# Optimization experiments

Measured on AMD Instinct MI355X. Metric: run time of the kernel, lower is better.

## Reference

```python
import jax, jax.numpy as jnp
import numpy as np

B, N, D = 2, 2048, 1024
H, WS = 16, 128  # num_heads, window_size
DH = D // H
HALF = WS // 2  # window is [i-HALF, i+HALF] inclusive -> 129 keys interior


def setup_inputs() -> dict:
    key = jax.random.key(0)
    ks = jax.random.split(key, 5)
    return {
        "x": jax.random.normal(ks[0], (B, N, D), dtype=jnp.float32),
        "Wqkv": jax.random.normal(ks[1], (D, 3 * D), dtype=jnp.float32) * 0.02,
        "bqkv": jax.random.normal(ks[2], (3 * D,), dtype=jnp.float32) * 0.02,
        "Wout": jax.random.normal(ks[3], (D, D), dtype=jnp.float32) * 0.02,
        "bout": jax.random.normal(ks[4], (D,), dtype=jnp.float32) * 0.02,
    }


def reference(x, Wqkv, bqkv, Wout, bout):
    b, n, d = x.shape
    scale = DH ** -0.5
    qkv = x @ Wqkv + bqkv  # [b, n, 3d]
    q, k, v = jnp.split(qkv, 3, axis=-1)
    # [b, n, d] -> [b, h, n, dh]
    def heads(t):
        return t.reshape(b, n, H, DH).transpose(0, 2, 1, 3)
    q, k, v = heads(q), heads(k), heads(v)
    scores = jnp.einsum("bhid,bhjd->bhij", q, k) * scale  # [b, h, n, n]
    # per-token window [max(0,i-HALF), min(n,i+HALF+1)) == |i-j| <= HALF
    idx = jnp.arange(n)
    band = jnp.abs(idx[:, None] - idx[None, :]) <= HALF  # [n, n]
    neg = jnp.asarray(jnp.finfo(scores.dtype).min, scores.dtype)
    scores = jnp.where(band[None, None], scores, neg)
    attn = jax.nn.softmax(scores, axis=-1)
    out = jnp.einsum("bhij,bhjd->bhid", attn, v)  # [b, h, n, dh]
    out = out.transpose(0, 2, 1, 3).reshape(b, n, d)
    return out @ Wout + bout
```

## Files before the change

kernel.cpp:

```cpp
#include <hip/hip_runtime.h>
#include <hip/hip_bf16.h>
#include <cstdint>
#include <cstddef>

#define BB 2
#define NN 2048
#define DD 1024
#define HH 16
#define DHH 64
#define SCALE 0.125f

typedef _Float16 f16x8 __attribute__((ext_vector_type(8)));
typedef _Float16 f16x4 __attribute__((ext_vector_type(4)));
typedef float f32x4 __attribute__((ext_vector_type(4)));

#define AS1(p) ((__attribute__((address_space(1))) void*)(p))
#define AS3(p) ((__attribute__((address_space(3))) void*)(p))

__global__ __launch_bounds__(256) void prep(const float* __restrict__ x, _Float16* __restrict__ x_h,
                                            const float* __restrict__ Wqkv, _Float16* __restrict__ Wqkv_t,
                                            const float* __restrict__ Wout, _Float16* __restrict__ Wout_t) {
    __shared__ float tile[32][33];
    int bx = blockIdx.x, tid = threadIdx.x;
    if (bx < 2048) {
        int i = bx * 2048 + tid * 8;
        f32x4 a = *(const f32x4*)(x + i);
        f32x4 b = *(const f32x4*)(x + i + 4);
        f16x8 o;
        o[0] = (_Float16)a[0]; o[1] = (_Float16)a[1]; o[2] = (_Float16)a[2]; o[3] = (_Float16)a[3];
        o[4] = (_Float16)b[0]; o[5] = (_Float16)b[1]; o[6] = (_Float16)b[2]; o[7] = (_Float16)b[3];
        *(f16x8*)(x_h + i) = o;
        return;
    }
    const float* in; _Float16* out; int C, tc, tr;
    if (bx < 5120) { int t = bx - 2048; C = 3 * DD; in = Wqkv; out = Wqkv_t; tc = t % 96; tr = t / 96; }
    else           { int t = bx - 5120; C = DD;     in = Wout; out = Wout_t; tc = t % 32; tr = t / 32; }
    int R = DD;
    int txx = tid & 31, ty = tid >> 5;
    int r0 = tr * 32, c0 = tc * 32;
#pragma unroll
    for (int i = 0; i < 32; i += 8)
        tile[ty + i][txx] = in[(size_t)(r0 + ty + i) * C + (c0 + txx)];
    __syncthreads();
#pragma unroll
    for (int i = 0; i < 32; i += 8)
        out[(size_t)(c0 + ty + i) * R + (r0 + txx)] = (_Float16)tile[txx][ty + i];
}

template <bool SWAP, int MT>
__device__ __forceinline__ void gemm_kloop(const _Float16* __restrict__ gA,
                                           const _Float16* __restrict__ gB,
                                           _Float16* lA, _Float16* lB,
                                           const _Float16* As, const _Float16* Bs,
                                           int wm, int wn, int llo, int lhi, int K,
                                           f32x4 acc[][MT > 4 ? MT : 4]) {
    for (int k0 = 0; k0 < K; k0 += 64) {
        __syncthreads();
#pragma unroll
        for (int p = 0; p < MT; ++p)
            __builtin_amdgcn_global_load_lds(AS1(gA + (size_t)p * 8 * K + k0), AS3(lA + p * 512), 16, 0, 0);
#pragma unroll
        for (int p = 0; p < 4; ++p)
            __builtin_amdgcn_global_load_lds(AS1(gB + (size_t)p * 8 * K + k0), AS3(lB + p * 512), 16, 0, 0);
        __syncthreads();

#pragma unroll
        for (int ks = 0; ks < 2; ++ks) {
            f16x8 af[MT], bf[4];
            int swz = (((ks * 4 + lhi) ^ (llo & 7)) * 8);
#pragma unroll
            for (int mt = 0; mt < MT; ++mt)
                af[mt] = *(const f16x8*)(As + (wm + mt * 16 + llo) * 64 + swz);
#pragma unroll
            for (int nt = 0; nt < 4; ++nt)
                bf[nt] = *(const f16x8*)(Bs + (wn + nt * 16 + llo) * 64 + swz);
            if (SWAP) {
#pragma unroll
                for (int nt = 0; nt < 4; ++nt)
#pragma unroll
                    for (int mt = 0; mt < MT; ++mt)
                        acc[nt][mt] = __builtin_amdgcn_mfma_f32_16x16x32_f16(bf[nt], af[mt], acc[nt][mt], 0, 0, 0);
            } else {
#pragma unroll
                for (int mt = 0; mt < MT; ++mt)
#pragma unroll
                    for (int nt = 0; nt < 4; ++nt)
                        acc[mt][nt] = __builtin_amdgcn_mfma_f32_16x16x32_f16(af[mt], bf[nt], acc[mt][nt], 0, 0, 0);
            }
        }
    }
}

template <bool SWAP>
__device__ __forceinline__ void qkv_body(const _Float16* __restrict__ A,
                                         const _Float16* __restrict__ Bt,
                                         const float* __restrict__ bias,
                                         _Float16* __restrict__ q_h,
                                         _Float16* __restrict__ k_h,
                                         _Float16* __restrict__ vt_h,
                                         _Float16* As, _Float16* Bs,
                                         int bm, int bn, int region) {
    (void)region;
    int tid = threadIdx.x;
    int wave = tid >> 6, lane = tid & 63;
    int llo = lane & 15, lhi = lane >> 4;
    int wm = (wave >> 2) * 128, wn = (wave & 3) * 64;
    int l8 = lane >> 3;
    int gchunk = ((lane & 7) ^ l8) * 8;

    int rAu = wm + (wave & 3) * 16;
    int rBu = (wave >> 1) * 64 + (wave & 1) * 16;
    const _Float16* gA = A + (size_t)(bm + rAu + l8) * DD + gchunk;
    const _Float16* gB = Bt + (size_t)(bn + rBu + l8) * DD + gchunk;
    _Float16* lA = As + rAu * 64 + lane * 8;
    _Float16* lB = Bs + rBu * 64 + lane * 8;

#define STA(H, C, T, U) __builtin_amdgcn_global_load_lds( \
        AS1(gA + (size_t)((H) * 64 + (C) * 8) * DD + (T) * 64), \
        AS3(lA + (U) * 16384 + ((H) * 64 + (C) * 8) * 64), 16, 0, 0)
#define STB(H, C, T, U) __builtin_amdgcn_global_load_lds( \
        AS1(gB + (size_t)((H) * 32 + (C) * 8) * DD + (T) * 64), \
        AS3(lB + (U) * 16384 + ((H) * 32 + (C) * 8) * 64), 16, 0, 0)
#define RDA(MT, KS, U) (*(const f16x8*)(As + (U) * 16384 + (wm + (MT) * 16 + llo) * 64 + ((((KS) * 4 + lhi) ^ (llo & 7)) * 8)))
#define RDB(NT, KS, U) (*(const f16x8*)(Bs + (U) * 16384 + (wn + (NT) * 16 + llo) * 64 + ((((KS) * 4 + lhi) ^ (llo & 7)) * 8)))
#define MM(MT, NT, KS) do { \
        if constexpr (SWAP) acc[NT][MT] = __builtin_amdgcn_mfma_f32_16x16x32_f16(bf[NT][KS], af[(MT) & 3][KS], acc[NT][MT], 0, 0, 0); \
        else acc[MT][NT] = __builtin_amdgcn_mfma_f32_16x16x32_f16(af[(MT) & 3][KS], bf[NT][KS], acc[MT][NT], 0, 0, 0); \
    } while (0)

    f32x4 acc[SWAP ? 4 : 8][SWAP ? 8 : 4] = {};
    f16x8 af[4][2], bf[4][2];

    STA(0, 0, 0, 0); STA(0, 1, 0, 0);
    STB(0, 0, 0, 0); STB(0, 1, 0, 0);
    STB(1, 0, 0, 0); STB(1, 1, 0, 0);
    STA(1, 0, 0, 0); STA(1, 1, 0, 0);
    asm volatile("s_waitcnt vmcnt(2)" ::: "memory");
    __builtin_amdgcn_s_barrier();

#pragma unroll 1
    for (int t = 0; t < 15; ++t) {
        int u = t & 1, nu = u ^ 1;
#pragma unroll
        for (int mt = 0; mt < 4; ++mt) { af[mt][0] = RDA(mt, 0, u); af[mt][1] = RDA(mt, 1, u); }
#pragma unroll
        for (int nt = 0; nt < 4; ++nt) { bf[nt][0] = RDB(nt, 0, u); bf[nt][1] = RDB(nt, 1, u); }
        STA(0, 0, t + 1, nu); STA(0, 1, t + 1, nu);
        STB(0, 0, t + 1, nu); STB(0, 1, t + 1, nu);
        STB(1, 0, t + 1, nu); STB(1, 1, t + 1, nu);
        __builtin_amdgcn_s_barrier();
        asm volatile("s_waitcnt lgkmcnt(0)" ::: "memory");
        __builtin_amdgcn_s_setprio(1);
#pragma unroll
        for (int ks = 0; ks < 2; ++ks)
#pragma unroll
            for (int mt = 0; mt < 4; ++mt) { MM(mt, 0, ks); MM(mt, 1, ks); MM(mt, 2, ks); MM(mt, 3, ks); }
        __builtin_amdgcn_s_setprio(0);
        asm volatile("s_waitcnt vmcnt(6)" ::: "memory");
        __builtin_amdgcn_s_barrier();
#pragma unroll
        for (int mt = 0; mt < 4; ++mt) { af[mt][0] = RDA(mt + 4, 0, u); af[mt][1] = RDA(mt + 4, 1, u); }
        STA(1, 0, t + 1, nu); STA(1, 1, t + 1, nu);
        __builtin_amdgcn_s_barrier();
        asm volatile("s_waitcnt lgkmcnt(0)" ::: "memory");
        __builtin_amdgcn_s_setprio(1);
#pragma unroll
        for (int ks = 0; ks < 2; ++ks)
#pragma unroll
            for (int mt = 4; mt < 8; ++mt) { MM(mt, 0, ks); MM(mt, 1, ks); MM(mt, 2, ks); MM(mt, 3, ks); }
        __builtin_amdgcn_s_setprio(0);
        asm volatile("s_waitcnt vmcnt(2)" ::: "memory");
        __builtin_amdgcn_s_barrier();
    }

    {
#pragma unroll
        for (int mt = 0; mt < 4; ++mt) { af[mt][0] = RDA(mt, 0, 1); af[mt][1] = RDA(mt, 1, 1); }
#pragma unroll
        for (int nt = 0; nt < 4; ++nt) { bf[nt][0] = RDB(nt, 0, 1); bf[nt][1] = RDB(nt, 1, 1); }
        asm volatile("s_waitcnt lgkmcnt(0)" ::: "memory");
        __builtin_amdgcn_s_setprio(1);
#pragma unroll
        for (int ks = 0; ks < 2; ++ks)
#pragma unroll
            for (int mt = 0; mt < 4; ++mt) { MM(mt, 0, ks); MM(mt, 1, ks); MM(mt, 2, ks); MM(mt, 3, ks); }
        __builtin_amdgcn_s_setprio(0);
        asm volatile("s_waitcnt vmcnt(0)" ::: "memory");
        __builtin_amdgcn_s_barrier();
#pragma unroll
        for (int mt = 0; mt < 4; ++mt) { af[mt][0] = RDA(mt + 4, 0, 1); af[mt][1] = RDA(mt + 4, 1, 1); }
        asm volatile("s_waitcnt lgkmcnt(0)" ::: "memory");
        __builtin_amdgcn_s_setprio(1);
#pragma unroll
        for (int ks = 0; ks < 2; ++ks)
#pragma unroll
            for (int mt = 4; mt < 8; ++mt) { MM(mt, 0, ks); MM(mt, 1, ks); MM(mt, 2, ks); MM(mt, 3, ks); }
        __builtin_amdgcn_s_setprio(0);
    }

    __builtin_amdgcn_s_barrier();
    _Float16* R = (wave < 4) ? (As + wave * 8192) : (Bs + (wave - 4) * 8192);
    int bq = bm >> 11;
    int nb = (bm & 2047) + wm;

    if constexpr (SWAP) {
#pragma unroll
        for (int nt = 0; nt < 4; ++nt) {
            int fb = nt * 16 + lhi * 4;
            f32x4 b4 = *(const f32x4*)(bias + bn + wn + fb);
            int chunk = fb >> 3, off = fb & 7;
#pragma unroll
            for (int mt = 0; mt < 8; ++mt) {
                int t = mt * 16 + llo;
                f16x4 v4;
#pragma unroll
                for (int r = 0; r < 4; ++r) v4[r] = (_Float16)(acc[nt][mt][r] + b4[r]);
                *(f16x4*)(R + t * 64 + ((chunk ^ (t & 7)) << 3) + off) = v4;
            }
        }
        asm volatile("s_waitcnt lgkmcnt(0)" ::: "memory");
        _Float16* dst0 = (region == 0 ? q_h : k_h);
        int cb = (bn & 1023) + wn;
#pragma unroll
        for (int it = 0; it < 16; ++it) {
            int t = it * 8 + l8;
            f16x8 v = *(const f16x8*)(R + t * 64 + (((lane & 7) ^ (t & 7)) << 3));
            *(f16x8*)(dst0 + (size_t)(bq * NN + nb + t) * DD + cb + (lane & 7) * 8) = v;
        }
    } else {
#pragma unroll
        for (int nt = 0; nt < 4; ++nt) {
            int f = nt * 16 + llo;
            float bv = bias[bn + wn + f];
#pragma unroll
            for (int mt = 0; mt < 8; ++mt) {
                int tb = mt * 16 + lhi * 4;
                int chunk = tb >> 3, off = tb & 7;
                int slot = (chunk & 8) | ((chunk & 7) ^ (f & 7));
                f16x4 v4;
#pragma unroll
                for (int r = 0; r < 4; ++r) v4[r] = (_Float16)(acc[mt][nt][r] + bv);
                *(f16x4*)(R + f * 128 + (slot << 3) + off) = v4;
            }
        }
        asm volatile("s_waitcnt lgkmcnt(0)" ::: "memory");
        int cb = (bn & 1023) + wn;
#pragma unroll
        for (int it = 0; it < 16; ++it) {
            int f = it * 4 + lhi;
            int chunk = llo;
            int slot = (chunk & 8) | ((chunk & 7) ^ (f & 7));
            f16x8 v = *(const f16x8*)(R + f * 128 + (slot << 3));
            int c = cb + f;
            int h = c >> 6, dh = c & 63;
            *(f16x8*)(vt_h + ((size_t)((bq * HH + h) * DHH + dh)) * NN + nb + chunk * 8) = v;
        }
    }
#undef STA
#undef STB
#undef RDA
#undef RDB
#undef MM
}

__global__ __launch_bounds__(512, 2) void gemm_qkv(const _Float16* __restrict__ A,
                                                   const _Float16* __restrict__ Bt,
                                                   const float* __restrict__ bias,
                                                   _Float16* __restrict__ q_h,
                                                   _Float16* __restrict__ k_h,
                                                   _Float16* __restrict__ vt_h) {
    __shared__ __align__(16) _Float16 As[2 * 16384];
    __shared__ __align__(16) _Float16 Bs[2 * 16384];
    int id = blockIdx.x;
    int xcd = id & 7, jj = id >> 3;
    int mtile = (xcd >> 1) * 4 + jj / 6;
    int ntile = (xcd & 1) * 6 + jj % 6;
    int bm = mtile * 256, bn = ntile * 256;
    int region = bn >> 10;
    if (region == 2)
        qkv_body<false>(A, Bt, bias, q_h, k_h, vt_h, As, Bs, bm, bn, region);
    else
        qkv_body<true>(A, Bt, bias, q_h, k_h, vt_h, As, Bs, bm, bn, region);
}

__global__ __launch_bounds__(256) void gemm_out(const _Float16* __restrict__ A,
                                                const _Float16* __restrict__ Bt,
                                                const float* __restrict__ bias,
                                                float* __restrict__ Cf) {
    const int K = DD, N = DD;
    __shared__ __align__(16) _Float16 As[128 * 64];
    __shared__ __align__(16) _Float16 Bs[128 * 64];
    int id = blockIdx.x;
    int xcd = id & 7, j = id >> 3;
    int bm = (xcd * 4 + (j >> 3)) * 128;
    int bn = (j & 7) * 128;
    int tid = threadIdx.x;
    int wave = tid >> 6, lane = tid & 63;
    int wm = (wave >> 1) * 64, wn = (wave & 1) * 64;
    int lhi = lane >> 4, llo = lane & 15;

    f32x4 acc[4][4] = {};

    int srow = wave * 32 + (lane >> 3);
    int scol = ((lane & 7) ^ (lane >> 3)) * 8;
    const _Float16* gA = A + (size_t)(bm + srow) * K + scol;
    const _Float16* gB = Bt + (size_t)(bn + srow) * K + scol;
    _Float16* lA = As + wave * 2048 + lane * 8;
    _Float16* lB = Bs + wave * 2048 + lane * 8;

    gemm_kloop<true, 4>(gA, gB, lA, lB, As, Bs, wm, wn, llo, lhi, K, acc);

#pragma unroll
    for (int nt = 0; nt < 4; ++nt) {
        int cbase = bn + wn + nt * 16 + lhi * 4;
        f32x4 b4 = *(const f32x4*)(bias + cbase);
#pragma unroll
        for (int mt = 0; mt < 4; ++mt) {
            int t = bm + wm + mt * 16 + llo;
            f32x4 v4;
#pragma unroll
            for (int r = 0; r < 4; ++r) v4[r] = acc[nt][mt][r] + b4[r];
            *(f32x4*)(Cf + (size_t)t * N + cbase) = v4;
        }
    }
}

#define KP 64
#define PP 200
#define VP 200
__global__ __launch_bounds__(256) void local_attn(const _Float16* __restrict__ q_h,
                                                  const _Float16* __restrict__ k_h,
                                                  const _Float16* __restrict__ vt_h,
                                                  _Float16* __restrict__ outh) {
    __shared__ __align__(16) _Float16 KsPs[64 * PP];
    __shared__ __align__(16) _Float16 Vt[64 * VP];
    _Float16* Ks = KsPs;
    _Float16* Ps = KsPs;
    int tid = threadIdx.x;
    int id = blockIdx.x;
    int xcd = id & 7, j = id >> 3;
    int i0 = (xcd * 4 + (j & 3)) * 64;
    int hb = j >> 2;
    int h = hb & 15, b = hb >> 4;

    int wave = tid >> 6, lane = tid & 63;
    int llo = lane & 15, lhi = lane >> 4;

    {
        int srow = lane >> 3;
        int chunk = ((lane & 7) ^ (lane >> 3)) * 8;
        const _Float16* kb = k_h + (size_t)(b * NN) * DD + h * DHH + chunk;
#pragma unroll
        for (int q = 0; q < 6; ++q) {
            int p = wave * 6 + q;
            int jj = i0 - 64 + p * 8 + srow;
            __builtin_amdgcn_global_load_lds(AS1(kb + (ptrdiff_t)jj * DD), AS3(Ks + p * 512 + lane * 8), 16, 0, 0);
        }
    }

    {
        const _Float16* vb = vt_h + (size_t)((b * HH + h) * DHH) * NN + (i0 - 64);
        for (int u = tid; u < 1536; u += 256) {
            int d = u / 24, c = u % 24;
            f16x8 vv = *(const f16x8*)(vb + (ptrdiff_t)d * NN + c * 8);
            *(f16x8*)(Vt + d * VP + c * 8) = vv;
        }
    }

    int qrow = wave * 16 + llo;
    int qi = i0 + qrow;
    const _Float16* qp = q_h + (size_t)(b * NN + qi) * DD + h * DHH;
    f16x8 qf0 = *(const f16x8*)(qp + lhi * 8);
    f16x8 qf1 = *(const f16x8*)(qp + 32 + lhi * 8);
    __syncthreads();

    float sc[12][4];
#pragma unroll
    for (int mt = 0; mt < 12; ++mt) {
        const _Float16* kr = Ks + (mt * 16 + llo) * 64;
        f16x8 kf0 = *(const f16x8*)(kr + ((lhi ^ (llo & 7)) * 8));
        f16x8 kf1 = *(const f16x8*)(kr + (((lhi + 4) ^ (llo & 7)) * 8));
        f32x4 a = {0.f, 0.f, 0.f, 0.f};
        a = __builtin_amdgcn_mfma_f32_16x16x32_f16(kf0, qf0, a, 0, 0, 0);
        a = __builtin_amdgcn_mfma_f32_16x16x32_f16(kf1, qf1, a, 0, 0, 0);
#pragma unroll
        for (int r = 0; r < 4; ++r) sc[mt][r] = a[r];
    }
    __syncthreads();

    float m = -1e30f;
#pragma unroll
    for (int mt = 0; mt < 12; ++mt)
#pragma unroll
        for (int r = 0; r < 4; ++r) {
            int sidx = mt * 16 + lhi * 4 + r;
            int jj = i0 - 64 + sidx;
            int dj = jj - qi;
            bool valid = (jj >= 0) && (jj < NN) && (dj <= 64) && (dj >= -64);
            float v = valid ? sc[mt][r] * SCALE : -1e30f;
            sc[mt][r] = v;
            m = fmaxf(m, v);
        }
    m = fmaxf(m, __shfl_xor(m, 16, 64));
    m = fmaxf(m, __shfl_xor(m, 32, 64));
    float l = 0.f;
#pragma unroll
    for (int mt = 0; mt < 12; ++mt)
#pragma unroll
        for (int r = 0; r < 4; ++r) {
            float e = __expf(sc[mt][r] - m);
            sc[mt][r] = e;
            l += e;
        }
    l += __shfl_xor(l, 16, 64);
    l += __shfl_xor(l, 32, 64);
    float invl = 1.f / l;

#pragma unroll
    for (int mt = 0; mt < 12; ++mt) {
        f16x4 pv;
#pragma unroll
        for (int r = 0; r < 4; ++r) pv[r] = (_Float16)(sc[mt][r] * invl);
        *(f16x4*)(Ps + qrow * PP + mt * 16 + lhi * 4) = pv;
    }
    __asm__ volatile("s_waitcnt lgkmcnt(0)" ::: "memory");

    f32x4 oacc[4] = {};
#pragma unroll
    for (int ks = 0; ks < 6; ++ks) {
        f16x8 pf = *(const f16x8*)(Ps + (wave * 16 + llo) * PP + ks * 32 + lhi * 8);
#pragma unroll
        for (int nt = 0; nt < 4; ++nt) {
            f16x8 vf = *(const f16x8*)(Vt + (nt * 16 + llo) * VP + ks * 32 + lhi * 8);
            oacc[nt] = __builtin_amdgcn_mfma_f32_16x16x32_f16(pf, vf, oacc[nt], 0, 0, 0);
        }
    }

    _Float16* orow = outh + (size_t)(b * NN) * DD + h * DHH;
#pragma unroll
    for (int nt = 0; nt < 4; ++nt)
#pragma unroll
        for (int r = 0; r < 4; ++r) {
            int q = wave * 16 + lhi * 4 + r;
            int d = nt * 16 + llo;
            orow[(size_t)(i0 + q) * DD + d] = (_Float16)oacc[nt][r];
        }
}

extern "C" void kernel_launch(void* const* d_in, const int* in_sizes, int n_in,
                              void* d_out, int out_size, void* d_ws, size_t ws_size,
                              hipStream_t stream) {
    const float* x    = (const float*)d_in[0];
    const float* Wqkv = (const float*)d_in[1];
    const float* bqkv = (const float*)d_in[2];
    const float* Wout = (const float*)d_in[3];
    const float* bout = (const float*)d_in[4];
    float* out = (float*)d_out;

    char* ws = (char*)d_ws;
    _Float16* x_h    = (_Float16*)(ws);
    _Float16* Wqkv_t = (_Float16*)(ws + (size_t)8  * 1024 * 1024);
    _Float16* Wout_t = (_Float16*)(ws + (size_t)14 * 1024 * 1024);
    _Float16* q_h    = (_Float16*)(ws + (size_t)16 * 1024 * 1024);
    _Float16* k_h    = (_Float16*)(ws + (size_t)24 * 1024 * 1024);
    _Float16* vt_h   = (_Float16*)(ws + (size_t)32 * 1024 * 1024);
    _Float16* attn_h = (_Float16*)(ws + (size_t)40 * 1024 * 1024);

    prep<<<6144, 256, 0, stream>>>(x, x_h, Wqkv, Wqkv_t, Wout, Wout_t);

    gemm_qkv<<<192, 512, 0, stream>>>(x_h, Wqkv_t, bqkv, q_h, k_h, vt_h);

    local_attn<<<1024, 256, 0, stream>>>(q_h, k_h, vt_h, attn_h);

    gemm_out<<<256, 256, 0, stream>>>(attn_h, Wout_t, bout, out);
}
```

Before: 151.8 us.

## Fuse all four stages into one cooperative persistent kernel with grid syncs

Replaces the four separate launches (prep, QKV GEMM, local attention, output GEMM) with one cooperative kernel of 256 blocks of 512 threads, using grid.sync between stages. This removes per-launch overhead and inter-kernel gaps. The attention tile is reshaped to 128 queries per block, with each wave working on only its 9 relevant key tiles instead of 12, and the output GEMM is retiled for 512 threads. The costs are fewer resident blocks during the element-wise and attention stages, idle blocks during the QKV stage (only 192 of 256 work), and the latency of grid-wide barriers.

```diff
diff --git a/kernel.cpp b/kernel.cpp
--- a/kernel.cpp
+++ b/kernel.cpp
@@ -1,7 +1,10 @@
 #include <hip/hip_runtime.h>
+#include <hip/hip_cooperative_groups.h>
 #include <hip/hip_bf16.h>
 #include <cstdint>
 #include <cstddef>
+
+namespace cg = cooperative_groups;
 
 #define BB 2
 #define NN 2048
@@ -16,80 +19,6 @@
 
 #define AS1(p) ((__attribute__((address_space(1))) void*)(p))
 #define AS3(p) ((__attribute__((address_space(3))) void*)(p))
-
-__global__ __launch_bounds__(256) void prep(const float* __restrict__ x, _Float16* __restrict__ x_h,
-                                            const float* __restrict__ Wqkv, _Float16* __restrict__ Wqkv_t,
-                                            const float* __restrict__ Wout, _Float16* __restrict__ Wout_t) {
-    __shared__ float tile[32][33];
-    int bx = blockIdx.x, tid = threadIdx.x;
-    if (bx < 2048) {
-        int i = bx * 2048 + tid * 8;
-        f32x4 a = *(const f32x4*)(x + i);
-        f32x4 b = *(const f32x4*)(x + i + 4);
-        f16x8 o;
-        o[0] = (_Float16)a[0]; o[1] = (_Float16)a[1]; o[2] = (_Float16)a[2]; o[3] = (_Float16)a[3];
-        o[4] = (_Float16)b[0]; o[5] = (_Float16)b[1]; o[6] = (_Float16)b[2]; o[7] = (_Float16)b[3];
-        *(f16x8*)(x_h + i) = o;
-        return;
-    }
-    const float* in; _Float16* out; int C, tc, tr;
-    if (bx < 5120) { int t = bx - 2048; C = 3 * DD; in = Wqkv; out = Wqkv_t; tc = t % 96; tr = t / 96; }
-    else           { int t = bx - 5120; C = DD;     in = Wout; out = Wout_t; tc = t % 32; tr = t / 32; }
-    int R = DD;
-    int txx = tid & 31, ty = tid >> 5;
-    int r0 = tr * 32, c0 = tc * 32;
-#pragma unroll
-    for (int i = 0; i < 32; i += 8)
-        tile[ty + i][txx] = in[(size_t)(r0 + ty + i) * C + (c0 + txx)];
-    __syncthreads();
-#pragma unroll
-    for (int i = 0; i < 32; i += 8)
-        out[(size_t)(c0 + ty + i) * R + (r0 + txx)] = (_Float16)tile[txx][ty + i];
-}
-
-template <bool SWAP, int MT>
-__device__ __forceinline__ void gemm_kloop(const _Float16* __restrict__ gA,
-                                           const _Float16* __restrict__ gB,
-                                           _Float16* lA, _Float16* lB,
-                                           const _Float16* As, const _Float16* Bs,
-                                           int wm, int wn, int llo, int lhi, int K,
-                                           f32x4 acc[][MT > 4 ? MT : 4]) {
-    for (int k0 = 0; k0 < K; k0 += 64) {
-        __syncthreads();
-#pragma unroll
-        for (int p = 0; p < MT; ++p)
-            __builtin_amdgcn_global_load_lds(AS1(gA + (size_t)p * 8 * K + k0), AS3(lA + p * 512), 16, 0, 0);
-#pragma unroll
-        for (int p = 0; p < 4; ++p)
-            __builtin_amdgcn_global_load_lds(AS1(gB + (size_t)p * 8 * K + k0), AS3(lB + p * 512), 16, 0, 0);
-        __syncthreads();
-
-#pragma unroll
-        for (int ks = 0; ks < 2; ++ks) {
-            f16x8 af[MT], bf[4];
-            int swz = (((ks * 4 + lhi) ^ (llo & 7)) * 8);
-#pragma unroll
-            for (int mt = 0; mt < MT; ++mt)
-                af[mt] = *(const f16x8*)(As + (wm + mt * 16 + llo) * 64 + swz);
-#pragma unroll
-            for (int nt = 0; nt < 4; ++nt)
-                bf[nt] = *(const f16x8*)(Bs + (wn + nt * 16 + llo) * 64 + swz);
-            if (SWAP) {
-#pragma unroll
-                for (int nt = 0; nt < 4; ++nt)
-#pragma unroll
-                    for (int mt = 0; mt < MT; ++mt)
-                        acc[nt][mt] = __builtin_amdgcn_mfma_f32_16x16x32_f16(bf[nt], af[mt], acc[nt][mt], 0, 0, 0);
-            } else {
-#pragma unroll
-                for (int mt = 0; mt < MT; ++mt)
-#pragma unroll
-                    for (int nt = 0; nt < 4; ++nt)
-                        acc[mt][nt] = __builtin_amdgcn_mfma_f32_16x16x32_f16(af[mt], bf[nt], acc[mt][nt], 0, 0, 0);
-            }
-        }
-    }
-}
 
 template <bool SWAP>
 __device__ __forceinline__ void qkv_body(const _Float16* __restrict__ A,
@@ -263,84 +192,20 @@
 #undef MM
 }
 
-__global__ __launch_bounds__(512, 2) void gemm_qkv(const _Float16* __restrict__ A,
-                                                   const _Float16* __restrict__ Bt,
-                                                   const float* __restrict__ bias,
-                                                   _Float16* __restrict__ q_h,
-                                                   _Float16* __restrict__ k_h,
-                                                   _Float16* __restrict__ vt_h) {
-    __shared__ __align__(16) _Float16 As[2 * 16384];
-    __shared__ __align__(16) _Float16 Bs[2 * 16384];
-    int id = blockIdx.x;
-    int xcd = id & 7, jj = id >> 3;
-    int mtile = (xcd >> 1) * 4 + jj / 6;
-    int ntile = (xcd & 1) * 6 + jj % 6;
-    int bm = mtile * 256, bn = ntile * 256;
-    int region = bn >> 10;
-    if (region == 2)
-        qkv_body<false>(A, Bt, bias, q_h, k_h, vt_h, As, Bs, bm, bn, region);
-    else
-        qkv_body<true>(A, Bt, bias, q_h, k_h, vt_h, As, Bs, bm, bn, region);
-}
-
-__global__ __launch_bounds__(256) void gemm_out(const _Float16* __restrict__ A,
-                                                const _Float16* __restrict__ Bt,
-                                                const float* __restrict__ bias,
-                                                float* __restrict__ Cf) {
-    const int K = DD, N = DD;
-    __shared__ __align__(16) _Float16 As[128 * 64];
-    __shared__ __align__(16) _Float16 Bs[128 * 64];
-    int id = blockIdx.x;
+#define PP2 168
+#define VP2 280
+__device__ __forceinline__ void attn_tile(int id, _Float16* smem,
+                                          const _Float16* __restrict__ q_h,
+                                          const _Float16* __restrict__ k_h,
+                                          const _Float16* __restrict__ vt_h,
+                                          _Float16* __restrict__ outh) {
+    _Float16* Ks = smem;
+    _Float16* Ps = smem;
+    _Float16* Vt = smem + 21504;
+    int tid = threadIdx.x;
     int xcd = id & 7, j = id >> 3;
-    int bm = (xcd * 4 + (j >> 3)) * 128;
-    int bn = (j & 7) * 128;
-    int tid = threadIdx.x;
-    int wave = tid >> 6, lane = tid & 63;
-    int wm = (wave >> 1) * 64, wn = (wave & 1) * 64;
-    int lhi = lane >> 4, llo = lane & 15;
-
-    f32x4 acc[4][4] = {};
-
-    int srow = wave * 32 + (lane >> 3);
-    int scol = ((lane & 7) ^ (lane >> 3)) * 8;
-    const _Float16* gA = A + (size_t)(bm + srow) * K + scol;
-    const _Float16* gB = Bt + (size_t)(bn + srow) * K + scol;
-    _Float16* lA = As + wave * 2048 + lane * 8;
-    _Float16* lB = Bs + wave * 2048 + lane * 8;
-
-    gemm_kloop<true, 4>(gA, gB, lA, lB, As, Bs, wm, wn, llo, lhi, K, acc);
-
-#pragma unroll
-    for (int nt = 0; nt < 4; ++nt) {
-        int cbase = bn + wn + nt * 16 + lhi * 4;
-        f32x4 b4 = *(const f32x4*)(bias + cbase);
-#pragma unroll
-        for (int mt = 0; mt < 4; ++mt) {
-            int t = bm + wm + mt * 16 + llo;
-            f32x4 v4;
-#pragma unroll
-            for (int r = 0; r < 4; ++r) v4[r] = acc[nt][mt][r] + b4[r];
-            *(f32x4*)(Cf + (size_t)t * N + cbase) = v4;
-        }
-    }
-}
-
-#define KP 64
-#define PP 200
-#define VP 200
-__global__ __launch_bounds__(256) void local_attn(const _Float16* __restrict__ q_h,
-                                                  const _Float16* __restrict__ k_h,
-                                                  const _Float16* __restrict__ vt_h,
-                                                  _Float16* __restrict__ outh) {
-    __shared__ __align__(16) _Float16 KsPs[64 * PP];
-    __shared__ __align__(16) _Float16 Vt[64 * VP];
-    _Float16* Ks = KsPs;
-    _Float16* Ps = KsPs;
-    int tid = threadIdx.x;
-    int id = blockIdx.x;
-    int xcd = id & 7, j = id >> 3;
-    int i0 = (xcd * 4 + (j & 3)) * 64;
-    int hb = j >> 2;
+    int i0 = (xcd * 2 + (j & 1)) * 128;
+    int hb = j >> 1;
     int h = hb & 15, b = hb >> 4;
 
     int wave = tid >> 6, lane = tid & 63;
@@ -351,8 +216,8 @@
         int chunk = ((lane & 7) ^ (lane >> 3)) * 8;
         const _Float16* kb = k_h + (size_t)(b * NN) * DD + h * DHH + chunk;
 #pragma unroll
-        for (int q = 0; q < 6; ++q) {
-            int p = wave * 6 + q;
+        for (int q = 0; q < 4; ++q) {
+            int p = wave * 4 + q;
             int jj = i0 - 64 + p * 8 + srow;
             __builtin_amdgcn_global_load_lds(AS1(kb + (ptrdiff_t)jj * DD), AS3(Ks + p * 512 + lane * 8), 16, 0, 0);
         }
@@ -360,10 +225,16 @@
 
     {
         const _Float16* vb = vt_h + (size_t)((b * HH + h) * DHH) * NN + (i0 - 64);
-        for (int u = tid; u < 1536; u += 256) {
-            int d = u / 24, c = u % 24;
+#pragma unroll
+        for (int u = tid; u < 2048; u += 512) {
+            int d = u >> 5, c = u & 31;
             f16x8 vv = *(const f16x8*)(vb + (ptrdiff_t)d * NN + c * 8);
-            *(f16x8*)(Vt + d * VP + c * 8) = vv;
+            *(f16x8*)(Vt + d * VP2 + c * 8) = vv;
+        }
+        if (tid < 192) {
+            int d = tid / 3, c = tid % 3;
+            f16x8 z = {};
+            *(f16x8*)(Vt + d * VP2 + 256 + c * 8) = z;
         }
     }
 
@@ -374,42 +245,42 @@
     f16x8 qf1 = *(const f16x8*)(qp + 32 + lhi * 8);
     __syncthreads();
 
-    float sc[12][4];
-#pragma unroll
-    for (int mt = 0; mt < 12; ++mt) {
-        const _Float16* kr = Ks + (mt * 16 + llo) * 64;
+    float sc[9][4];
+#pragma unroll
+    for (int mtl = 0; mtl < 9; ++mtl) {
+        const _Float16* kr = Ks + ((wave + mtl) * 16 + llo) * 64;
         f16x8 kf0 = *(const f16x8*)(kr + ((lhi ^ (llo & 7)) * 8));
         f16x8 kf1 = *(const f16x8*)(kr + (((lhi + 4) ^ (llo & 7)) * 8));
         f32x4 a = {0.f, 0.f, 0.f, 0.f};
         a = __builtin_amdgcn_mfma_f32_16x16x32_f16(kf0, qf0, a, 0, 0, 0);
         a = __builtin_amdgcn_mfma_f32_16x16x32_f16(kf1, qf1, a, 0, 0, 0);
 #pragma unroll
-        for (int r = 0; r < 4; ++r) sc[mt][r] = a[r];
+        for (int r = 0; r < 4; ++r) sc[mtl][r] = a[r];
     }
     __syncthreads();
 
     float m = -1e30f;
 #pragma unroll
-    for (int mt = 0; mt < 12; ++mt)
+    for (int mtl = 0; mtl < 9; ++mtl)
 #pragma unroll
         for (int r = 0; r < 4; ++r) {
-            int sidx = mt * 16 + lhi * 4 + r;
+            int sidx = (wave + mtl) * 16 + lhi * 4 + r;
             int jj = i0 - 64 + sidx;
             int dj = jj - qi;
             bool valid = (jj >= 0) && (jj < NN) && (dj <= 64) && (dj >= -64);
-            float v = valid ? sc[mt][r] * SCALE : -1e30f;
-            sc[mt][r] = v;
+            float v = valid ? sc[mtl][r] * SCALE : -1e30f;
+            sc[mtl][r] = v;
             m = fmaxf(m, v);
         }
     m = fmaxf(m, __shfl_xor(m, 16, 64));
     m = fmaxf(m, __shfl_xor(m, 32, 64));
     float l = 0.f;
 #pragma unroll
-    for (int mt = 0; mt < 12; ++mt)
+    for (int mtl = 0; mtl < 9; ++mtl)
 #pragma unroll
         for (int r = 0; r < 4; ++r) {
-            float e = __expf(sc[mt][r] - m);
-            sc[mt][r] = e;
+            float e = __expf(sc[mtl][r] - m);
+            sc[mtl][r] = e;
             l += e;
         }
     l += __shfl_xor(l, 16, 64);
@@ -417,21 +288,25 @@
     float invl = 1.f / l;
 
 #pragma unroll
-    for (int mt = 0; mt < 12; ++mt) {
+    for (int mtl = 0; mtl < 9; ++mtl) {
         f16x4 pv;
 #pragma unroll
-        for (int r = 0; r < 4; ++r) pv[r] = (_Float16)(sc[mt][r] * invl);
-        *(f16x4*)(Ps + qrow * PP + mt * 16 + lhi * 4) = pv;
+        for (int r = 0; r < 4; ++r) pv[r] = (_Float16)(sc[mtl][r] * invl);
+        *(f16x4*)(Ps + qrow * PP2 + mtl * 16 + lhi * 4) = pv;
+    }
+    {
+        f16x4 z4 = {};
+        *(f16x4*)(Ps + qrow * PP2 + 144 + lhi * 4) = z4;
     }
     __asm__ volatile("s_waitcnt lgkmcnt(0)" ::: "memory");
 
     f32x4 oacc[4] = {};
 #pragma unroll
-    for (int ks = 0; ks < 6; ++ks) {
-        f16x8 pf = *(const f16x8*)(Ps + (wave * 16 + llo) * PP + ks * 32 + lhi * 8);
+    for (int ks = 0; ks < 5; ++ks) {
+        f16x8 pf = *(const f16x8*)(Ps + qrow * PP2 + ks * 32 + lhi * 8);
 #pragma unroll
         for (int nt = 0; nt < 4; ++nt) {
-            f16x8 vf = *(const f16x8*)(Vt + (nt * 16 + llo) * VP + ks * 32 + lhi * 8);
+            f16x8 vf = *(const f16x8*)(Vt + (nt * 16 + llo) * VP2 + wave * 16 + ks * 32 + lhi * 8);
             oacc[nt] = __builtin_amdgcn_mfma_f32_16x16x32_f16(pf, vf, oacc[nt], 0, 0, 0);
         }
     }
@@ -445,6 +320,135 @@
             int d = nt * 16 + llo;
             orow[(size_t)(i0 + q) * DD + d] = (_Float16)oacc[nt][r];
         }
+}
+
+__global__ __launch_bounds__(512, 2) void fused(const float* __restrict__ x,
+                                                const float* __restrict__ Wqkv,
+                                                const float* __restrict__ bqkv,
+                                                const float* __restrict__ Wout,
+                                                const float* __restrict__ bout,
+                                                float* __restrict__ out,
+                                                _Float16* __restrict__ x_h,
+                                                _Float16* __restrict__ Wqkv_t,
+                                                _Float16* __restrict__ Wout_t,
+                                                _Float16* __restrict__ q_h,
+                                                _Float16* __restrict__ k_h,
+                                                _Float16* __restrict__ vt_h,
+                                                _Float16* __restrict__ attn_h) {
+    __shared__ __align__(16) _Float16 smem[65536];
+    cg::grid_group grid = cg::this_grid();
+    int bid = blockIdx.x, tid = threadIdx.x;
+
+    {
+        for (int u = bid * 512 + tid; u < 524288; u += 256 * 512) {
+            int i = u * 8;
+            f32x4 a = *(const f32x4*)(x + i);
+            f32x4 b = *(const f32x4*)(x + i + 4);
+            f16x8 o;
+            o[0] = (_Float16)a[0]; o[1] = (_Float16)a[1]; o[2] = (_Float16)a[2]; o[3] = (_Float16)a[3];
+            o[4] = (_Float16)b[0]; o[5] = (_Float16)b[1]; o[6] = (_Float16)b[2]; o[7] = (_Float16)b[3];
+            *(f16x8*)(x_h + i) = o;
+        }
+        float* ftile = (float*)smem;
+        int half = tid >> 8, t2 = tid & 255;
+        int txx = t2 & 31, ty = t2 >> 5;
+        float* T = ftile + half * (32 * 33);
+        for (int it = 0; it < 8; ++it) {
+            int u = bid * 16 + it * 2 + half;
+            const float* in; _Float16* outp; int C, tc, tr;
+            if (u < 3072) { C = 3 * DD; in = Wqkv; outp = Wqkv_t; tc = u % 96; tr = u / 96; }
+            else { int v = u - 3072; C = DD; in = Wout; outp = Wout_t; tc = v % 32; tr = v / 32; }
+            int r0 = tr * 32, c0 = tc * 32;
+            __syncthreads();
+#pragma unroll
+            for (int i = 0; i < 32; i += 8)
+                T[(ty + i) * 33 + txx] = in[(size_t)(r0 + ty + i) * C + (c0 + txx)];
+            __syncthreads();
+#pragma unroll
+            for (int i = 0; i < 32; i += 8)
+                outp[(size_t)(c0 + ty + i) * DD + (r0 + txx)] = (_Float16)T[txx * 33 + (ty + i)];
+        }
+    }
+    grid.sync();
+
+    if (bid < 192) {
+        int xcd = bid & 7, jj = bid >> 3;
+        int mtile = (xcd >> 1) * 4 + jj / 6;
+        int ntile = (xcd & 1) * 6 + jj % 6;
+        int bm = mtile * 256, bn = ntile * 256;
+        int region = bn >> 10;
+        if (region == 2)
+            qkv_body<false>(x_h, Wqkv_t, bqkv, q_h, k_h, vt_h, smem, smem + 32768, bm, bn, region);
+        else
+            qkv_body<true>(x_h, Wqkv_t, bqkv, q_h, k_h, vt_h, smem, smem + 32768, bm, bn, region);
+    }
+    grid.sync();
+
+    for (int it = 0; it < 2; ++it) {
+        __syncthreads();
+        attn_tile(bid + it * 256, smem, q_h, k_h, vt_h, attn_h);
+    }
+    grid.sync();
+
+    {
+        _Float16* OAs = smem;
+        _Float16* OBs = smem + 8192;
+        int xcd = bid & 7, j = bid >> 3;
+        int bm = (xcd * 4 + (j >> 3)) * 128;
+        int bn = (j & 7) * 128;
+        int wave = tid >> 6, lane = tid & 63;
+        int wm = (wave >> 2) * 64, wn = (wave & 3) * 32;
+        int lhi = lane >> 4, llo = lane & 15;
+
+        f32x4 acc[2][4] = {};
+
+        int srow = wave * 16 + (lane >> 3);
+        int scol = ((lane & 7) ^ (lane >> 3)) * 8;
+        const _Float16* gA = attn_h + (size_t)(bm + srow) * DD + scol;
+        const _Float16* gB = Wout_t + (size_t)(bn + srow) * DD + scol;
+        _Float16* lA = OAs + wave * 1024 + lane * 8;
+        _Float16* lB = OBs + wave * 1024 + lane * 8;
+
+        for (int k0 = 0; k0 < DD; k0 += 64) {
+            __syncthreads();
+#pragma unroll
+            for (int p = 0; p < 2; ++p) {
+                __builtin_amdgcn_global_load_lds(AS1(gA + (size_t)p * 8 * DD + k0), AS3(lA + p * 512), 16, 0, 0);
+                __builtin_amdgcn_global_load_lds(AS1(gB + (size_t)p * 8 * DD + k0), AS3(lB + p * 512), 16, 0, 0);
+            }
+            __syncthreads();
+#pragma unroll
+            for (int ks = 0; ks < 2; ++ks) {
+                f16x8 af[4], bf[2];
+                int swz = (((ks * 4 + lhi) ^ (llo & 7)) * 8);
+#pragma unroll
+                for (int mt = 0; mt < 4; ++mt)
+                    af[mt] = *(const f16x8*)(OAs + (wm + mt * 16 + llo) * 64 + swz);
+#pragma unroll
+                for (int nt = 0; nt < 2; ++nt)
+                    bf[nt] = *(const f16x8*)(OBs + (wn + nt * 16 + llo) * 64 + swz);
+#pragma unroll
+                for (int nt = 0; nt < 2; ++nt)
+#pragma unroll
+                    for (int mt = 0; mt < 4; ++mt)
+                        acc[nt][mt] = __builtin_amdgcn_mfma_f32_16x16x32_f16(bf[nt], af[mt], acc[nt][mt], 0, 0, 0);
+            }
+        }
+
+#pragma unroll
+        for (int nt = 0; nt < 2; ++nt) {
+            int cbase = bn + wn + nt * 16 + lhi * 4;
+            f32x4 b4 = *(const f32x4*)(bout + cbase);
+#pragma unroll
+            for (int mt = 0; mt < 4; ++mt) {
+                int t = bm + wm + mt * 16 + llo;
+                f32x4 v4;
+#pragma unroll
+                for (int r = 0; r < 4; ++r) v4[r] = acc[nt][mt][r] + b4[r];
+                *(f32x4*)(out + (size_t)t * DD + cbase) = v4;
+            }
+        }
+    }
 }
 
 extern "C" void kernel_launch(void* const* d_in, const int* in_sizes, int n_in,
@@ -466,11 +470,8 @@
     _Float16* vt_h   = (_Float16*)(ws + (size_t)32 * 1024 * 1024);
     _Float16* attn_h = (_Float16*)(ws + (size_t)40 * 1024 * 1024);
 
-    prep<<<6144, 256, 0, stream>>>(x, x_h, Wqkv, Wqkv_t, Wout, Wout_t);
-
-    gemm_qkv<<<192, 512, 0, stream>>>(x_h, Wqkv_t, bqkv, q_h, k_h, vt_h);
-
-    local_attn<<<1024, 256, 0, stream>>>(q_h, k_h, vt_h, attn_h);
-
-    gemm_out<<<256, 256, 0, stream>>>(attn_h, Wout_t, bout, out);
+    void* args[] = {(void*)&x, (void*)&Wqkv, (void*)&bqkv, (void*)&Wout, (void*)&bout,
+                    (void*)&out, (void*)&x_h, (void*)&Wqkv_t, (void*)&Wout_t,
+                    (void*)&q_h, (void*)&k_h, (void*)&vt_h, (void*)&attn_h};
+    hipLaunchCooperativeKernel((void*)fused, dim3(256), dim3(512), args, 0, stream);
 }
```

Result: slower. 258.6 us (+70.3%).

## Retile QKV GEMM to 256x192 tiles so grid fills 256 CUs

Applied to the files above, without the earlier changes.

The QKV projection GEMM moves from 256x256 tiles (192 blocks) to 256x192 tiles (256 blocks), so every CU on the MI355X gets one block and the partial-wave tail goes away. Each wave now owns 48 output columns (3 MFMA n-tiles), and the B-tile load pattern and LDS staging are rewritten to match. Because a tile can now straddle the q/k/v boundaries, the epilogue picks the destination per column, and V columns are written with scattered scalar stores instead of the swizzled transposed path. The cost is lower arithmetic intensity per block and uncoalesced V-transpose writes.

```diff
diff --git a/kernel.cpp b/kernel.cpp
--- a/kernel.cpp
+++ b/kernel.cpp
@@ -91,178 +91,6 @@
     }
 }
 
-template <bool SWAP>
-__device__ __forceinline__ void qkv_body(const _Float16* __restrict__ A,
-                                         const _Float16* __restrict__ Bt,
-                                         const float* __restrict__ bias,
-                                         _Float16* __restrict__ q_h,
-                                         _Float16* __restrict__ k_h,
-                                         _Float16* __restrict__ vt_h,
-                                         _Float16* As, _Float16* Bs,
-                                         int bm, int bn, int region) {
-    (void)region;
-    int tid = threadIdx.x;
-    int wave = tid >> 6, lane = tid & 63;
-    int llo = lane & 15, lhi = lane >> 4;
-    int wm = (wave >> 2) * 128, wn = (wave & 3) * 64;
-    int l8 = lane >> 3;
-    int gchunk = ((lane & 7) ^ l8) * 8;
-
-    int rAu = wm + (wave & 3) * 16;
-    int rBu = (wave >> 1) * 64 + (wave & 1) * 16;
-    const _Float16* gA = A + (size_t)(bm + rAu + l8) * DD + gchunk;
-    const _Float16* gB = Bt + (size_t)(bn + rBu + l8) * DD + gchunk;
-    _Float16* lA = As + rAu * 64 + lane * 8;
-    _Float16* lB = Bs + rBu * 64 + lane * 8;
-
-#define STA(H, C, T, U) __builtin_amdgcn_global_load_lds( \
-        AS1(gA + (size_t)((H) * 64 + (C) * 8) * DD + (T) * 64), \
-        AS3(lA + (U) * 16384 + ((H) * 64 + (C) * 8) * 64), 16, 0, 0)
-#define STB(H, C, T, U) __builtin_amdgcn_global_load_lds( \
-        AS1(gB + (size_t)((H) * 32 + (C) * 8) * DD + (T) * 64), \
-        AS3(lB + (U) * 16384 + ((H) * 32 + (C) * 8) * 64), 16, 0, 0)
-#define RDA(MT, KS, U) (*(const f16x8*)(As + (U) * 16384 + (wm + (MT) * 16 + llo) * 64 + ((((KS) * 4 + lhi) ^ (llo & 7)) * 8)))
-#define RDB(NT, KS, U) (*(const f16x8*)(Bs + (U) * 16384 + (wn + (NT) * 16 + llo) * 64 + ((((KS) * 4 + lhi) ^ (llo & 7)) * 8)))
-#define MM(MT, NT, KS) do { \
-        if constexpr (SWAP) acc[NT][MT] = __builtin_amdgcn_mfma_f32_16x16x32_f16(bf[NT][KS], af[(MT) & 3][KS], acc[NT][MT], 0, 0, 0); \
-        else acc[MT][NT] = __builtin_amdgcn_mfma_f32_16x16x32_f16(af[(MT) & 3][KS], bf[NT][KS], acc[MT][NT], 0, 0, 0); \
-    } while (0)
-
-    f32x4 acc[SWAP ? 4 : 8][SWAP ? 8 : 4] = {};
-    f16x8 af[4][2], bf[4][2];
-
-    STA(0, 0, 0, 0); STA(0, 1, 0, 0);
-    STB(0, 0, 0, 0); STB(0, 1, 0, 0);
-    STB(1, 0, 0, 0); STB(1, 1, 0, 0);
-    STA(1, 0, 0, 0); STA(1, 1, 0, 0);
-    asm volatile("s_waitcnt vmcnt(2)" ::: "memory");
-    __builtin_amdgcn_s_barrier();
-
-#pragma unroll 1
-    for (int t = 0; t < 15; ++t) {
-        int u = t & 1, nu = u ^ 1;
-#pragma unroll
-        for (int mt = 0; mt < 4; ++mt) { af[mt][0] = RDA(mt, 0, u); af[mt][1] = RDA(mt, 1, u); }
-#pragma unroll
-        for (int nt = 0; nt < 4; ++nt) { bf[nt][0] = RDB(nt, 0, u); bf[nt][1] = RDB(nt, 1, u); }
-        STA(0, 0, t + 1, nu); STA(0, 1, t + 1, nu);
-        STB(0, 0, t + 1, nu); STB(0, 1, t + 1, nu);
-        STB(1, 0, t + 1, nu); STB(1, 1, t + 1, nu);
-        __builtin_amdgcn_s_barrier();
-        asm volatile("s_waitcnt lgkmcnt(0)" ::: "memory");
-        __builtin_amdgcn_s_setprio(1);
-#pragma unroll
-        for (int ks = 0; ks < 2; ++ks)
-#pragma unroll
-            for (int mt = 0; mt < 4; ++mt) { MM(mt, 0, ks); MM(mt, 1, ks); MM(mt, 2, ks); MM(mt, 3, ks); }
-        __builtin_amdgcn_s_setprio(0);
-        asm volatile("s_waitcnt vmcnt(6)" ::: "memory");
-        __builtin_amdgcn_s_barrier();
-#pragma unroll
-        for (int mt = 0; mt < 4; ++mt) { af[mt][0] = RDA(mt + 4, 0, u); af[mt][1] = RDA(mt + 4, 1, u); }
-        STA(1, 0, t + 1, nu); STA(1, 1, t + 1, nu);
-        __builtin_amdgcn_s_barrier();
-        asm volatile("s_waitcnt lgkmcnt(0)" ::: "memory");
-        __builtin_amdgcn_s_setprio(1);
-#pragma unroll
-        for (int ks = 0; ks < 2; ++ks)
-#pragma unroll
-            for (int mt = 4; mt < 8; ++mt) { MM(mt, 0, ks); MM(mt, 1, ks); MM(mt, 2, ks); MM(mt, 3, ks); }
-        __builtin_amdgcn_s_setprio(0);
-        asm volatile("s_waitcnt vmcnt(2)" ::: "memory");
-        __builtin_amdgcn_s_barrier();
-    }
-
-    {
-#pragma unroll
-        for (int mt = 0; mt < 4; ++mt) { af[mt][0] = RDA(mt, 0, 1); af[mt][1] = RDA(mt, 1, 1); }
-#pragma unroll
-        for (int nt = 0; nt < 4; ++nt) { bf[nt][0] = RDB(nt, 0, 1); bf[nt][1] = RDB(nt, 1, 1); }
-        asm volatile("s_waitcnt lgkmcnt(0)" ::: "memory");
-        __builtin_amdgcn_s_setprio(1);
-#pragma unroll
-        for (int ks = 0; ks < 2; ++ks)
-#pragma unroll
-            for (int mt = 0; mt < 4; ++mt) { MM(mt, 0, ks); MM(mt, 1, ks); MM(mt, 2, ks); MM(mt, 3, ks); }
-        __builtin_amdgcn_s_setprio(0);
-        asm volatile("s_waitcnt vmcnt(0)" ::: "memory");
-        __builtin_amdgcn_s_barrier();
-#pragma unroll
-        for (int mt = 0; mt < 4; ++mt) { af[mt][0] = RDA(mt + 4, 0, 1); af[mt][1] = RDA(mt + 4, 1, 1); }
-        asm volatile("s_waitcnt lgkmcnt(0)" ::: "memory");
-        __builtin_amdgcn_s_setprio(1);
-#pragma unroll
-        for (int ks = 0; ks < 2; ++ks)
-#pragma unroll
-            for (int mt = 4; mt < 8; ++mt) { MM(mt, 0, ks); MM(mt, 1, ks); MM(mt, 2, ks); MM(mt, 3, ks); }
-        __builtin_amdgcn_s_setprio(0);
-    }
-
-    __builtin_amdgcn_s_barrier();
-    _Float16* R = (wave < 4) ? (As + wave * 8192) : (Bs + (wave - 4) * 8192);
-    int bq = bm >> 11;
-    int nb = (bm & 2047) + wm;
-
-    if constexpr (SWAP) {
-#pragma unroll
-        for (int nt = 0; nt < 4; ++nt) {
-            int fb = nt * 16 + lhi * 4;
-            f32x4 b4 = *(const f32x4*)(bias + bn + wn + fb);
-            int chunk = fb >> 3, off = fb & 7;
-#pragma unroll
-            for (int mt = 0; mt < 8; ++mt) {
-                int t = mt * 16 + llo;
-                f16x4 v4;
-#pragma unroll
-                for (int r = 0; r < 4; ++r) v4[r] = (_Float16)(acc[nt][mt][r] + b4[r]);
-                *(f16x4*)(R + t * 64 + ((chunk ^ (t & 7)) << 3) + off) = v4;
-            }
-        }
-        asm volatile("s_waitcnt lgkmcnt(0)" ::: "memory");
-        _Float16* dst0 = (region == 0 ? q_h : k_h);
-        int cb = (bn & 1023) + wn;
-#pragma unroll
-        for (int it = 0; it < 16; ++it) {
-            int t = it * 8 + l8;
-            f16x8 v = *(const f16x8*)(R + t * 64 + (((lane & 7) ^ (t & 7)) << 3));
-            *(f16x8*)(dst0 + (size_t)(bq * NN + nb + t) * DD + cb + (lane & 7) * 8) = v;
-        }
-    } else {
-#pragma unroll
-        for (int nt = 0; nt < 4; ++nt) {
-            int f = nt * 16 + llo;
-            float bv = bias[bn + wn + f];
-#pragma unroll
-            for (int mt = 0; mt < 8; ++mt) {
-                int tb = mt * 16 + lhi * 4;
-                int chunk = tb >> 3, off = tb & 7;
-                int slot = (chunk & 8) | ((chunk & 7) ^ (f & 7));
-                f16x4 v4;
-#pragma unroll
-                for (int r = 0; r < 4; ++r) v4[r] = (_Float16)(acc[mt][nt][r] + bv);
-                *(f16x4*)(R + f * 128 + (slot << 3) + off) = v4;
-            }
-        }
-        asm volatile("s_waitcnt lgkmcnt(0)" ::: "memory");
-        int cb = (bn & 1023) + wn;
-#pragma unroll
-        for (int it = 0; it < 16; ++it) {
-            int f = it * 4 + lhi;
-            int chunk = llo;
-            int slot = (chunk & 8) | ((chunk & 7) ^ (f & 7));
-            f16x8 v = *(const f16x8*)(R + f * 128 + (slot << 3));
-            int c = cb + f;
-            int h = c >> 6, dh = c & 63;
-            *(f16x8*)(vt_h + ((size_t)((bq * HH + h) * DHH + dh)) * NN + nb + chunk * 8) = v;
-        }
-    }
-#undef STA
-#undef STB
-#undef RDA
-#undef RDB
-#undef MM
-}
-
 __global__ __launch_bounds__(512, 2) void gemm_qkv(const _Float16* __restrict__ A,
                                                    const _Float16* __restrict__ Bt,
                                                    const float* __restrict__ bias,
@@ -270,17 +98,164 @@
                                                    _Float16* __restrict__ k_h,
                                                    _Float16* __restrict__ vt_h) {
     __shared__ __align__(16) _Float16 As[2 * 16384];
-    __shared__ __align__(16) _Float16 Bs[2 * 16384];
+    __shared__ __align__(16) _Float16 Bs[2 * 12288];
     int id = blockIdx.x;
     int xcd = id & 7, jj = id >> 3;
-    int mtile = (xcd >> 1) * 4 + jj / 6;
-    int ntile = (xcd & 1) * 6 + jj % 6;
-    int bm = mtile * 256, bn = ntile * 256;
-    int region = bn >> 10;
-    if (region == 2)
-        qkv_body<false>(A, Bt, bias, q_h, k_h, vt_h, As, Bs, bm, bn, region);
-    else
-        qkv_body<true>(A, Bt, bias, q_h, k_h, vt_h, As, Bs, bm, bn, region);
+    int mtile = (xcd >> 1) * 4 + (jj >> 3);
+    int ntile = (xcd & 1) * 8 + (jj & 7);
+    int bm = mtile * 256, bn = ntile * 192;
+
+    int tid = threadIdx.x;
+    int wave = tid >> 6, lane = tid & 63;
+    int llo = lane & 15, lhi = lane >> 4;
+    int wm = (wave >> 2) * 128, wn = (wave & 3) * 48;
+    int l8 = lane >> 3;
+    int gchunk = ((lane & 7) ^ l8) * 8;
+
+    int rAu = wm + (wave & 3) * 16;
+    const _Float16* gA = A + (size_t)(bm + rAu + l8) * DD + gchunk;
+    _Float16* lA = As + rAu * 64 + lane * 8;
+    const _Float16* gB = Bt + (size_t)(bn + wave * 8 + l8) * DD + gchunk;
+    _Float16* lB = Bs + wave * 512 + lane * 8;
+
+#define STA(H, C, T, U) __builtin_amdgcn_global_load_lds( \
+        AS1(gA + (size_t)((H) * 64 + (C) * 8) * DD + (T) * 64), \
+        AS3(lA + (U) * 16384 + ((H) * 64 + (C) * 8) * 64), 16, 0, 0)
+#define STB(G, T, U) __builtin_amdgcn_global_load_lds( \
+        AS1(gB + (size_t)((G) * 64) * DD + (T) * 64), \
+        AS3(lB + (U) * 12288 + (G) * 4096), 16, 0, 0)
+#define RDA(MT, KS, U) (*(const f16x8*)(As + (U) * 16384 + (wm + (MT) * 16 + llo) * 64 + ((((KS) * 4 + lhi) ^ (llo & 7)) * 8)))
+#define RDB(NT, KS, U) (*(const f16x8*)(Bs + (U) * 12288 + (wn + (NT) * 16 + llo) * 64 + ((((KS) * 4 + lhi) ^ (llo & 7)) * 8)))
+#define MM(MT, NT, KS) \
+        acc[NT][MT] = __builtin_amdgcn_mfma_f32_16x16x32_f16(bf[NT][KS], af[(MT) & 3][KS], acc[NT][MT], 0, 0, 0)
+
+    f32x4 acc[3][8] = {};
+    f16x8 af[4][2], bf[3][2];
+
+    STA(0, 0, 0, 0); STA(0, 1, 0, 0);
+    STB(0, 0, 0); STB(1, 0, 0); STB(2, 0, 0);
+    STA(1, 0, 0, 0); STA(1, 1, 0, 0);
+    asm volatile("s_waitcnt vmcnt(2)" ::: "memory");
+    __builtin_amdgcn_s_barrier();
+
+#pragma unroll 1
+    for (int t = 0; t < 15; ++t) {
+        int u = t & 1, nu = u ^ 1;
+#pragma unroll
+        for (int mt = 0; mt < 4; ++mt) { af[mt][0] = RDA(mt, 0, u); af[mt][1] = RDA(mt, 1, u); }
+#pragma unroll
+        for (int nt = 0; nt < 3; ++nt) { bf[nt][0] = RDB(nt, 0, u); bf[nt][1] = RDB(nt, 1, u); }
+        STA(0, 0, t + 1, nu); STA(0, 1, t + 1, nu);
+        STB(0, t + 1, nu); STB(1, t + 1, nu); STB(2, t + 1, nu);
+        __builtin_amdgcn_s_barrier();
+        asm volatile("s_waitcnt lgkmcnt(0)" ::: "memory");
+        __builtin_amdgcn_s_setprio(1);
+#pragma unroll
+        for (int ks = 0; ks < 2; ++ks)
+#pragma unroll
+            for (int mt = 0; mt < 4; ++mt) { MM(mt, 0, ks); MM(mt, 1, ks); MM(mt, 2, ks); }
+        __builtin_amdgcn_s_setprio(0);
+        asm volatile("s_waitcnt vmcnt(5)" ::: "memory");
+        __builtin_amdgcn_s_barrier();
+#pragma unroll
+        for (int mt = 0; mt < 4; ++mt) { af[mt][0] = RDA(mt + 4, 0, u); af[mt][1] = RDA(mt + 4, 1, u); }
+        STA(1, 0, t + 1, nu); STA(1, 1, t + 1, nu);
+        __builtin_amdgcn_s_barrier();
+        asm volatile("s_waitcnt lgkmcnt(0)" ::: "memory");
+        __builtin_amdgcn_s_setprio(1);
+#pragma unroll
+        for (int ks = 0; ks < 2; ++ks)
+#pragma unroll
+            for (int mt = 4; mt < 8; ++mt) { MM(mt, 0, ks); MM(mt, 1, ks); MM(mt, 2, ks); }
+        __builtin_amdgcn_s_setprio(0);
+        asm volatile("s_waitcnt vmcnt(2)" ::: "memory");
+        __builtin_amdgcn_s_barrier();
+    }
+
+    {
+#pragma unroll
+        for (int mt = 0; mt < 4; ++mt) { af[mt][0] = RDA(mt, 0, 1); af[mt][1] = RDA(mt, 1, 1); }
+#pragma unroll
+        for (int nt = 0; nt < 3; ++nt) { bf[nt][0] = RDB(nt, 0, 1); bf[nt][1] = RDB(nt, 1, 1); }
+        asm volatile("s_waitcnt lgkmcnt(0)" ::: "memory");
+        __builtin_amdgcn_s_setprio(1);
+#pragma unroll
+        for (int ks = 0; ks < 2; ++ks)
+#pragma unroll
+            for (int mt = 0; mt < 4; ++mt) { MM(mt, 0, ks); MM(mt, 1, ks); MM(mt, 2, ks); }
+        __builtin_amdgcn_s_setprio(0);
+        asm volatile("s_waitcnt vmcnt(0)" ::: "memory");
+        __builtin_amdgcn_s_barrier();
+#pragma unroll
+        for (int mt = 0; mt < 4; ++mt) { af[mt][0] = RDA(mt + 4, 0, 1); af[mt][1] = RDA(mt + 4, 1, 1); }
+        asm volatile("s_waitcnt lgkmcnt(0)" ::: "memory");
+        __builtin_amdgcn_s_setprio(1);
+#pragma unroll
+        for (int ks = 0; ks < 2; ++ks)
+#pragma unroll
+            for (int mt = 4; mt < 8; ++mt) { MM(mt, 0, ks); MM(mt, 1, ks); MM(mt, 2, ks); }
+        __builtin_amdgcn_s_setprio(0);
+    }
+
+    __builtin_amdgcn_s_barrier();
+    _Float16* R = (wave < 4) ? (As + wave * 6144) : (Bs + (wave - 4) * 6144);
+    int bq = bm >> 11;
+    int nb = (bm & 2047) + wm;
+    int cwb = bn + wn;
+
+#pragma unroll
+    for (int nt = 0; nt < 3; ++nt) {
+        int fb = nt * 16 + lhi * 4;
+        f32x4 b4 = *(const f32x4*)(bias + cwb + fb);
+        int chunk = fb >> 3, off = fb & 7;
+#pragma unroll
+        for (int mt = 0; mt < 8; ++mt) {
+            int t = mt * 16 + llo;
+            f16x4 v4;
+#pragma unroll
+            for (int r = 0; r < 4; ++r) v4[r] = (_Float16)(acc[nt][mt][r] + b4[r]);
+            *(f16x4*)(R + t * 48 + ((chunk + t) % 6) * 8 + off) = v4;
+        }
+    }
+    asm volatile("s_waitcnt lgkmcnt(0)" ::: "memory");
+#pragma unroll
+    for (int it = 0; it < 16; ++it) {
+        int t = it * 8 + l8;
+        int c = lane & 7;
+        if (c < 6) {
+            int col = cwb + c * 8;
+            int rg = col >> 10;
+            if (rg < 2) {
+                f16x8 v = *(const f16x8*)(R + t * 48 + ((c + t) % 6) * 8);
+                _Float16* dst = rg ? k_h : q_h;
+                *(f16x8*)(dst + (size_t)(bq * NN + nb + t) * DD + (col & 1023)) = v;
+            }
+        }
+    }
+#pragma unroll
+    for (int nt = 0; nt < 3; ++nt) {
+        int colbase = cwb + nt * 16;
+        if ((colbase >> 10) == 2) {
+            int fb = nt * 16 + lhi * 4;
+            f32x4 b4 = *(const f32x4*)(bias + cwb + fb);
+#pragma unroll
+            for (int r = 0; r < 4; ++r) {
+                int c1023 = (colbase + lhi * 4 + r) & 1023;
+                int h = c1023 >> 6, dh = c1023 & 63;
+                _Float16* vb = vt_h + ((size_t)((bq * HH + h) * DHH + dh)) * NN;
+#pragma unroll
+                for (int mt = 0; mt < 8; ++mt) {
+                    int n = nb + mt * 16 + llo;
+                    vb[n] = (_Float16)(acc[nt][mt][r] + b4[r]);
+                }
+            }
+        }
+    }
+#undef STA
+#undef STB
+#undef RDA
+#undef RDB
+#undef MM
 }
 
 __global__ __launch_bounds__(256) void gemm_out(const _Float16* __restrict__ A,
@@ -468,7 +443,7 @@
 
     prep<<<6144, 256, 0, stream>>>(x, x_h, Wqkv, Wqkv_t, Wout, Wout_t);
 
-    gemm_qkv<<<192, 512, 0, stream>>>(x_h, Wqkv_t, bqkv, q_h, k_h, vt_h);
+    gemm_qkv<<<256, 512, 0, stream>>>(x_h, Wqkv_t, bqkv, q_h, k_h, vt_h);
 
     local_attn<<<1024, 256, 0, stream>>>(q_h, k_h, vt_h, attn_h);
 
```

Result: no change. 150.9 us (-0.6%).
